# Performance work log

Hardware: AMD Instinct MI355X
Metric: run time of the kernel (lower is better)

## Reference

```python
import jax, jax.numpy as jnp
import numpy as np
import math

N_COARSE, N_FINE = 8192, 32768
DEC_DIM, ENC_DIM, OUT_DIM, K = 256, 128, 128, 16
LN_EPS = 1e-5


def setup_inputs() -> dict:
    key = jax.random.key(0)
    ks = jax.random.split(key, 16)
    s = lambda fan_in: 1.0 / math.sqrt(fan_in)
    return {
        "decoder_features": jax.random.normal(ks[0], (N_COARSE, DEC_DIM), jnp.float32),
        "decoder_pos": jax.random.normal(ks[1], (N_COARSE, 3), jnp.float32),
        "encoder_features": jax.random.normal(ks[2], (N_FINE, ENC_DIM), jnp.float32),
        "encoder_pos": jax.random.normal(ks[3], (N_FINE, 3), jnp.float32),
        "encoder_labels": jax.random.randint(ks[4], (N_FINE,), 0, 13, jnp.int64),
        # params (torch nn.Linear default init scale)
        "Wq": jax.random.uniform(ks[5], (DEC_DIM, ENC_DIM), jnp.float32, -s(ENC_DIM), s(ENC_DIM)),
        "bq": jnp.zeros((DEC_DIM,), jnp.float32),
        "Wk": jax.random.uniform(ks[6], (DEC_DIM, DEC_DIM), jnp.float32, -s(DEC_DIM), s(DEC_DIM)),
        "bk": jnp.zeros((DEC_DIM,), jnp.float32),
        "Wv": jax.random.uniform(ks[7], (DEC_DIM, DEC_DIM), jnp.float32, -s(DEC_DIM), s(DEC_DIM)),
        "bv": jnp.zeros((DEC_DIM,), jnp.float32),
        "W1": jax.random.uniform(ks[8], (OUT_DIM, DEC_DIM + ENC_DIM), jnp.float32, -s(DEC_DIM + ENC_DIM), s(DEC_DIM + ENC_DIM)),
        "b1": jnp.zeros((OUT_DIM,), jnp.float32),
        "W2": jax.random.uniform(ks[9], (OUT_DIM, OUT_DIM), jnp.float32, -s(OUT_DIM), s(OUT_DIM)),
        "b2": jnp.zeros((OUT_DIM,), jnp.float32),
        "ln_g": jnp.ones((OUT_DIM,), jnp.float32),
        "ln_b": jnp.zeros((OUT_DIM,), jnp.float32),
    }


def _knn_indices(encoder_pos, decoder_pos, k):
    # For each fine (encoder) point, k nearest coarse (decoder) points.
    # squared distances [N_fine, N_coarse]
    d2 = (
        jnp.sum(encoder_pos * encoder_pos, axis=1, keepdims=True)
        - 2.0 * encoder_pos @ decoder_pos.T
        + jnp.sum(decoder_pos * decoder_pos, axis=1)[None, :]
    )
    _, idx = jax.lax.top_k(-d2, k)  # [N_fine, K]
    return idx


def reference(decoder_features, decoder_pos, encoder_features, encoder_pos,
              encoder_labels, Wq, bq, Wk, bk, Wv, bv, W1, b1, W2, b2, ln_g, ln_b):
    idx = _knn_indices(encoder_pos, decoder_pos, K)            # [Nf, K]
    nbr = decoder_features[idx]                                 # [Nf, K, Dd]
    query = encoder_features @ Wq.T + bq                        # [Nf, Dd]
    keys = nbr @ Wk.T + bk                                      # [Nf, K, Dd]
    values = nbr @ Wv.T + bv                                    # [Nf, K, Dd]
    scores = jnp.einsum('nd,nkd->nk', query, keys) / math.sqrt(DEC_DIM)
    # segment softmax over edges grouped by fine target == softmax over K
    weights = jax.nn.softmax(scores, axis=-1)                   # [Nf, K]
    agg = jnp.einsum('nk,nkd->nd', weights, values)             # [Nf, Dd]
    combined = jnp.concatenate([agg, encoder_features], axis=-1)
    h = jax.nn.relu(combined @ W1.T + b1)
    up = h @ W2.T + b2                                          # [Nf, out]
    mu = jnp.mean(up, axis=-1, keepdims=True)
    var = jnp.var(up, axis=-1, keepdims=True)
    out = (up - mu) * jax.lax.rsqrt(var + LN_EPS) * ln_g + ln_b
    # dropout is identity in eval mode
    return (out, encoder_pos, encoder_labels)
```

## Files before the change

kernel.cpp:

```cpp
#include <hip/hip_runtime.h>
#include <hip/hip_bf16.h>

typedef __hip_bfloat16 bf16;
typedef unsigned short u16;
typedef float f32x2 __attribute__((ext_vector_type(2)));

#define NC 8192
#define NF 32768
#define KNN 16
#define FMAXV 3.402823466e+38f

__device__ __forceinline__ float bfbits2f(u16 u){
  union { unsigned u; float f; } x; x.u = ((unsigned)u) << 16; return x.f;
}
__device__ __forceinline__ float asfloat(unsigned u){
  union { unsigned u; float f; } x; x.u = u; return x.f;
}
__device__ __forceinline__ f32x2 pk_fma(f32x2 a, f32x2 b, f32x2 c){
  f32x2 d;
  asm("v_pk_fma_f32 %0, %1, %2, %3" : "=v"(d) : "v"(a), "v"(b), "v"(c));
  return d;
}

__global__ __launch_bounds__(256) void k_pw(const float* __restrict__ dpos,
                                            const float* __restrict__ W1,
                                            const float* __restrict__ W2,
                                            float4* __restrict__ posP,
                                            float4* __restrict__ W1eSa,
                                            float4* __restrict__ W1eSb,
                                            float4* __restrict__ W2Sa,
                                            float4* __restrict__ W2Sb,
                                            const float* __restrict__ Wk,
                                            const float* __restrict__ Wv,
                                            const float* __restrict__ Wq,
                                            const float* __restrict__ bk,
                                            const float* __restrict__ bv,
                                            const float* __restrict__ bq,
                                            float* __restrict__ WkqS,
                                            float* __restrict__ WvuS,
                                            float* __restrict__ bkq,
                                            float* __restrict__ bvu,
                                            float* __restrict__ wbq,
                                            float* __restrict__ sbq,
                                            const float* __restrict__ epos,
                                            const int* __restrict__ lab,
                                            float* __restrict__ out){
  __shared__ float partial[256];
  __shared__ float red[256];
  int gb = blockIdx.x, t = threadIdx.x;
  if (gb >= 1092){
    int gid = (gb - 1092) * 256 + t;
    if (gid < NF){
      float* op = out + (size_t)NF * 128;
      op[gid * 3 + 0] = epos[gid * 3 + 0];
      op[gid * 3 + 1] = epos[gid * 3 + 1];
      op[gid * 3 + 2] = epos[gid * 3 + 2];
      out[(size_t)NF * 128 + (size_t)NF * 3 + gid] = (float)lab[gid];
    }
    return;
  }
  if (gb >= 1028){
    int g = (gb - 1028) * 256 + t;
    if (g < 4096){
      const float2* dp2 = (const float2*)(dpos + (size_t)g * 6);
      float2 a = dp2[0], b = dp2[1], c = dp2[2];
      float x0 = a.x, y0 = a.y, z0 = b.x;
      float x1 = b.y, y1 = c.x, z1 = c.y;
      float dd0 = __fadd_rn(__fadd_rn(__fmul_rn(x0,x0), __fmul_rn(y0,y0)), __fmul_rn(z0,z0));
      float dd1 = __fadd_rn(__fadd_rn(__fmul_rn(x1,x1), __fmul_rn(y1,y1)), __fmul_rn(z1,z1));
      posP[g * 2]     = make_float4(x0, x1, y0, y1);
      posP[g * 2 + 1] = make_float4(z0, z1, dd0 * 0.5f, dd1 * 0.5f);
    } else if (g >= 8192 && g < 10240){
      int f = g - 8192; int c4 = f >> 6, jg = f & 63;
      W1eSa[f] = ((const float4*)(W1 + (size_t)(2 * jg) * 384 + 256))[c4];
    } else if (g >= 10240 && g < 12288){
      int f = g - 10240; int c4 = f >> 6, jg = f & 63;
      W1eSb[f] = ((const float4*)(W1 + (size_t)(2 * jg + 1) * 384 + 256))[c4];
    } else if (g >= 12288 && g < 14336){
      int f = g - 12288; int c4 = f >> 6, jg = f & 63;
      W2Sa[f] = ((const float4*)(W2 + (size_t)(2 * jg) * 128))[c4];
    } else if (g >= 14336 && g < 16384){
      int f = g - 14336; int c4 = f >> 6, jg = f & 63;
      W2Sb[f] = ((const float4*)(W2 + (size_t)(2 * jg + 1) * 128))[c4];
    }
    return;
  }
  int B = gb;
  int csel = B >> 2, tch = B & 3;
  int o = (t & 63) + tch * 64;
  int q = t >> 6;
  int j0 = q * 64;
  if (csel < 128){
    int c = csel;
    float acc = 0.f;
    for (int j = j0; j < j0 + 64; ++j)
      acc = fmaf(Wk[(size_t)j * 256 + o], Wq[(size_t)j * 128 + c], acc);
    partial[t] = acc;
    if (tch == 0) red[t] = bk[t] * Wq[(size_t)t * 128 + c];
    __syncthreads();
    if (t < 64){
      float a = partial[t] + partial[t + 64] + partial[t + 128] + partial[t + 192];
      WkqS[(size_t)((o >> 2) * 128 + c) * 4 + (o & 3)] = a;
    }
    if (tch == 0){
      for (int s = 128; s > 0; s >>= 1){ if (t < s) red[t] += red[t + s]; __syncthreads(); }
      if (t == 0) bkq[c] = red[0];
    }
  } else if (csel < 256){
    int h = csel - 128;
    float acc = 0.f;
    for (int j = j0; j < j0 + 64; ++j)
      acc = fmaf(Wv[(size_t)j * 256 + o], W1[(size_t)h * 384 + j], acc);
    partial[t] = acc;
    if (tch == 0) red[t] = bv[t] * W1[(size_t)h * 384 + t];
    __syncthreads();
    if (t < 64){
      float a = partial[t] + partial[t + 64] + partial[t + 128] + partial[t + 192];
      WvuS[(size_t)((o >> 2) * 128 + h) * 4 + (o & 3)] = a;
    }
    if (tch == 0){
      for (int s = 128; s > 0; s >>= 1){ if (t < s) red[t] += red[t + s]; __syncthreads(); }
      if (t == 0) bvu[h] = red[0];
    }
  } else {
    float acc = 0.f;
    for (int j = j0; j < j0 + 64; ++j)
      acc = fmaf(Wk[(size_t)j * 256 + o], bq[j], acc);
    partial[t] = acc;
    if (tch == 0) red[t] = bk[t] * bq[t];
    __syncthreads();
    if (t < 64){
      float a = partial[t] + partial[t + 64] + partial[t + 128] + partial[t + 192];
      wbq[o] = a;
    }
    if (tch == 0){
      for (int s = 128; s > 0; s >>= 1){ if (t < s) red[t] += red[t + s]; __syncthreads(); }
      if (t == 0) sbq[0] = red[0];
    }
  }
}

__global__ __launch_bounds__(256) void k_dk(const float* __restrict__ df,
                                            const float4* __restrict__ WkqS,
                                            const float4* __restrict__ WvuS,
                                            const float* __restrict__ bkq,
                                            const float* __restrict__ bvu,
                                            const float* __restrict__ wbq,
                                            const float* __restrict__ sbq,
                                            bf16* __restrict__ Zd, bf16* __restrict__ Ud,
                                            float* __restrict__ bqK,
                                            const float* __restrict__ epos,
                                            const float4* __restrict__ posP,
                                            int* __restrict__ knnI){
  __shared__ float dpart[8][32];
  __shared__ float smin[8 * 64];
  __shared__ float tauLDS[8];
  __shared__ int   cntL[8][4];
  __shared__ float lval[8][4][64];
  __shared__ int   lidx[8][4][64];

  int g = blockIdx.x, t = threadIdx.x;
  int m = g % 5, q5 = g / 5;
  if (m == 4){
    int g0 = q5 * 8;
    int half = __builtin_amdgcn_readfirstlane(t >> 7);
    int c = t & 127;
    const float4* W = half ? WvuS : WkqS;
    float acc[8];
    #pragma unroll
    for (int p = 0; p < 8; ++p) acc[p] = 0.f;
    for (int j4 = 0; j4 < 64; ++j4){
      float4 w = W[j4 * 128 + c];
      #pragma unroll
      for (int p = 0; p < 8; ++p){
        float4 a = ((const float4*)(df + (size_t)(g0 + p) * 256))[j4];
        acc[p] += w.x*a.x + w.y*a.y + w.z*a.z + w.w*a.w;
      }
    }
    float bias = half ? bvu[c] : bkq[c];
    bf16* dst = half ? Ud : Zd;
    #pragma unroll
    for (int p = 0; p < 8; ++p)
      dst[(size_t)(g0 + p) * 128 + c] = __float2bfloat16(acc[p] + bias);
    {
      int r = t >> 5, seg = t & 31;
      float s = 0.f;
      const float* dr = df + (size_t)(g0 + r) * 256 + seg * 8;
      const float* wq = wbq + seg * 8;
      #pragma unroll
      for (int e = 0; e < 8; ++e) s = fmaf(dr[e], wq[e], s);
      dpart[r][seg] = s;
    }
    __syncthreads();
    if (t < 8){
      float s = sbq[0];
      #pragma unroll
      for (int seg = 0; seg < 32; ++seg) s += dpart[t][seg];
      bqK[g0 + t] = s;
    }
    return;
  }

  int kb = q5 * 4 + m;
  int lane = t & 63, w = t >> 6;
  int n0 = kb * 8;
  f32x2 nex2[8], ney2[8], nez2[8];
  #pragma unroll
  for (int p = 0; p < 8; ++p){
    float nx = -epos[(n0 + p) * 3 + 0];
    float ny = -epos[(n0 + p) * 3 + 1];
    float nz = -epos[(n0 + p) * 3 + 2];
    nex2[p].x = nx; nex2[p].y = nx;
    ney2[p].x = ny; ney2[p].y = ny;
    nez2[p].x = nz; nez2[p].y = nz;
  }
  const float4* base = posP + w * 2048;

  f32x2 vmin2[8];
  #pragma unroll
  for (int p = 0; p < 8; ++p){ vmin2[p].x = FMAXV; vmin2[p].y = FMAXV; }
  #pragma unroll 4
  for (int s = 0; s < 16; ++s){
    int q2 = (s * 64 + lane) * 2;
    float4 XY = base[q2], ZW = base[q2 + 1];
    f32x2 X = {XY.x, XY.y}, Y = {XY.z, XY.w}, Z = {ZW.x, ZW.y}, W = {ZW.z, ZW.w};
    #pragma unroll
    for (int p = 0; p < 8; ++p){
      f32x2 v2 = pk_fma(nex2[p], X, W);
      v2 = pk_fma(ney2[p], Y, v2);
      v2 = pk_fma(nez2[p], Z, v2);
      vmin2[p].x = fminf(vmin2[p].x, v2.x);
      vmin2[p].y = fminf(vmin2[p].y, v2.y);
    }
  }
  float vmin[8];
  #pragma unroll
  for (int p = 0; p < 8; ++p) vmin[p] = fminf(vmin2[p].x, vmin2[p].y);

  #pragma unroll
  for (int k = 2; k <= 64; k <<= 1){
    #pragma unroll
    for (int j = k >> 1; j > 0; j >>= 1){
      bool keepmin = ((lane & j) == 0) == ((lane & k) == 0);
      #pragma unroll
      for (int p = 0; p < 8; ++p){
        float pv = __shfl_xor(vmin[p], j);
        vmin[p] = keepmin ? fminf(vmin[p], pv) : fmaxf(vmin[p], pv);
      }
    }
  }
  if (lane < 16){
    #pragma unroll
    for (int p = 0; p < 8; ++p) smin[p * 64 + w * 16 + lane] = vmin[p];
  }
  __syncthreads();

  {
    int src = (lane & 16) ? (lane ^ 15) : lane;
    float v0 = smin[(w * 2 + 0) * 64 + src];
    float v1 = smin[(w * 2 + 1) * 64 + src];
    #pragma unroll
    for (int j = 16; j > 0; j >>= 1){
      bool keepmin = ((lane & 32) == 0) == ((lane & j) == 0);
      float p0 = __shfl_xor(v0, j); v0 = keepmin ? fminf(v0, p0) : fmaxf(v0, p0);
      float p1 = __shfl_xor(v1, j); v1 = keepmin ? fminf(v1, p1) : fmaxf(v1, p1);
    }
    #pragma unroll
    for (int j = 32; j > 0; j >>= 1){
      bool keepmin = ((lane & j) == 0);
      float p0 = __shfl_xor(v0, j); v0 = keepmin ? fminf(v0, p0) : fmaxf(v0, p0);
      float p1 = __shfl_xor(v1, j); v1 = keepmin ? fminf(v1, p1) : fmaxf(v1, p1);
    }
    if (lane == 16){ tauLDS[w * 2] = v0; tauLDS[w * 2 + 1] = v1; }
  }
  __syncthreads();
  float tau0[8];
  #pragma unroll
  for (int p = 0; p < 8; ++p) tau0[p] = tauLDS[p];

  unsigned long long lmlt = (1ull << lane) - 1ull;
  int cnt[8] = {0,0,0,0,0,0,0,0};
  #pragma unroll 2
  for (int s = 0; s < 16; ++s){
    int q = s * 64 + lane;
    float4 XY = base[q * 2], ZW = base[q * 2 + 1];
    f32x2 X = {XY.x, XY.y}, Y = {XY.z, XY.w}, Z = {ZW.x, ZW.y}, W = {ZW.z, ZW.w};
    int cand0 = w * 2048 + q * 2;
    #pragma unroll
    for (int p = 0; p < 8; ++p){
      f32x2 v2 = pk_fma(nex2[p], X, W);
      v2 = pk_fma(ney2[p], Y, v2);
      v2 = pk_fma(nez2[p], Z, v2);
      bool h0 = v2.x <= tau0[p];
      bool h1 = v2.y <= tau0[p];
      unsigned long long m0 = __ballot(h0);
      unsigned long long m1 = __ballot(h1);
      if (m0 | m1){
        int base0 = cnt[p];
        int c0 = (int)__popcll(m0);
        if (h0){
          int s0 = base0 + (int)__popcll(m0 & lmlt);
          if (s0 < 64){ lval[p][w][s0] = v2.x; lidx[p][w][s0] = cand0; }
        }
        if (h1){
          int s1 = base0 + c0 + (int)__popcll(m1 & lmlt);
          if (s1 < 64){ lval[p][w][s1] = v2.y; lidx[p][w][s1] = cand0 + 1; }
        }
        cnt[p] = base0 + c0 + (int)__popcll(m1);
      }
    }
  }
  if (lane == 0){
    #pragma unroll
    for (int p = 0; p < 8; ++p) cntL[p][w] = (cnt[p] > 64) ? 64 : cnt[p];
  }
  __syncthreads();

  {
    int p0 = w * 2, p1 = w * 2 + 1;
    int nA = n0 + p0, nB = n0 + p1;
    int cA0 = cntL[p0][0], cA1 = cntL[p0][1], cA2 = cntL[p0][2], cA3 = cntL[p0][3];
    int cB0 = cntL[p1][0], cB1 = cntL[p1][1], cB2 = cntL[p1][2], cB3 = cntL[p1][3];
    int oA1 = cA0, oA2 = oA1 + cA1, oA3 = oA2 + cA2; int totA = oA3 + cA3; if (totA > 64) totA = 64;
    int oB1 = cB0, oB2 = oB1 + cB1, oB3 = oB2 + cB2; int totB = oB3 + cB3; if (totB > 64) totB = 64;
    int segA = (lane >= oA1) + (lane >= oA2) + (lane >= oA3);
    int segB = (lane >= oB1) + (lane >= oB2) + (lane >= oB3);
    int basA = segA == 0 ? 0 : (segA == 1 ? oA1 : (segA == 2 ? oA2 : oA3));
    int basB = segB == 0 ? 0 : (segB == 1 ? oB1 : (segB == 2 ? oB2 : oB3));
    float va = (lane < totA) ? lval[p0][segA][lane - basA] : FMAXV;
    int   ia = (lane < totA) ? lidx[p0][segA][lane - basA] : 0x7fffffff;
    float vb = (lane < totB) ? lval[p1][segB][lane - basB] : FMAXV;
    int   ib = (lane < totB) ? lidx[p1][segB][lane - basB] : 0x7fffffff;

    #pragma unroll
    for (int k = 2; k <= 16; k <<= 1){
      #pragma unroll
      for (int j = k >> 1; j > 0; j >>= 1){
        bool keepmin = ((lane & k) == 0) == ((lane & j) == 0);
        { float pv = __shfl_xor(va, j); int pid = __shfl_xor(ia, j);
          bool pl = (pv < va) || (pv == va && pid < ia);
          if (keepmin ? pl : !pl){ va = pv; ia = pid; } }
        { float pv = __shfl_xor(vb, j); int pid = __shfl_xor(ib, j);
          bool pl = (pv < vb) || (pv == vb && pid < ib);
          if (keepmin ? pl : !pl){ vb = pv; ib = pid; } }
      }
    }
    { float pv = __shfl_xor(va, 16); int pid = __shfl_xor(ia, 16);
      if ((pv < va) || (pv == va && pid < ia)){ va = pv; ia = pid; } }
    { float pv = __shfl_xor(vb, 16); int pid = __shfl_xor(ib, 16);
      if ((pv < vb) || (pv == vb && pid < ib)){ vb = pv; ib = pid; } }
    #pragma unroll
    for (int j = 8; j > 0; j >>= 1){
      bool keepmin = ((lane & 32) == 0) == ((lane & j) == 0);
      { float pv = __shfl_xor(va, j); int pid = __shfl_xor(ia, j);
        bool pl = (pv < va) || (pv == va && pid < ia);
        if (keepmin ? pl : !pl){ va = pv; ia = pid; } }
      { float pv = __shfl_xor(vb, j); int pid = __shfl_xor(ib, j);
        bool pl = (pv < vb) || (pv == vb && pid < ib);
        if (keepmin ? pl : !pl){ vb = pv; ib = pid; } }
    }
    { float pv = __shfl_xor(va, 32); int pid = __shfl_xor(ia, 32);
      if ((pv < va) || (pv == va && pid < ia)){ va = pv; ia = pid; } }
    { float pv = __shfl_xor(vb, 32); int pid = __shfl_xor(ib, 32);
      if ((pv < vb) || (pv == vb && pid < ib)){ vb = pv; ib = pid; } }

    if (lane < 16){
      knnI[(size_t)nA * 16 + lane] = ia;
      knnI[(size_t)nB * 16 + lane] = ib;
    }
  }
}

__global__ __launch_bounds__(256) void k_amlp(const int* __restrict__ knnI,
                                              const bf16* __restrict__ Zd,
                                              const bf16* __restrict__ Ud,
                                              const float* __restrict__ bqK,
                                              const float* __restrict__ ef,
                                              const float4* __restrict__ W1eSa,
                                              const float4* __restrict__ W1eSb,
                                              const float* __restrict__ b1,
                                              const float4* __restrict__ W2Sa,
                                              const float4* __restrict__ W2Sb,
                                              const float* __restrict__ b2,
                                              const float* __restrict__ lng, const float* __restrict__ lnb,
                                              float* __restrict__ out){
  __shared__ float haggL[16 * 128];
  __shared__ float hbuf[16 * 128];
  __shared__ float ubuf[16 * 128];
  __shared__ float stats[32];
  int t = threadIdx.x;
  int n0 = blockIdx.x * 16;
  int lane = t & 63, w = t >> 6;

  {
    int kk = lane & 15;
    int pp = w * 4 + (lane >> 4);
    int n = n0 + pp;
    int ik = knnI[(size_t)n * 16 + kk];
    float bz = bqK[ik];
    const float4* e4 = (const float4*)(ef + (size_t)n * 128 + kk * 8);
    float4 ea = e4[0], eb = e4[1];
    int gbase = lane & 48;
    int ikk[16];
    #pragma unroll
    for (int k2 = 0; k2 < 16; ++k2) ikk[k2] = __shfl(ik, gbase | k2);
    float qv[16];
    {
      uint4 zb[8];
      #pragma unroll
      for (int k2 = 0; k2 < 8; ++k2) zb[k2] = *(const uint4*)((const u16*)Zd + (size_t)ikk[k2] * 128 + kk * 8);
      #pragma unroll
      for (int k2 = 0; k2 < 8; ++k2){
        uint4 z = zb[k2];
        float s;
        s = ea.x * asfloat(z.x << 16);
        s = fmaf(ea.y, asfloat(z.x & 0xffff0000u), s);
        s = fmaf(ea.z, asfloat(z.y << 16), s);
        s = fmaf(ea.w, asfloat(z.y & 0xffff0000u), s);
        s = fmaf(eb.x, asfloat(z.z << 16), s);
        s = fmaf(eb.y, asfloat(z.z & 0xffff0000u), s);
        s = fmaf(eb.z, asfloat(z.w << 16), s);
        s = fmaf(eb.w, asfloat(z.w & 0xffff0000u), s);
        qv[k2] = s;
      }
      #pragma unroll
      for (int k2 = 0; k2 < 8; ++k2) zb[k2] = *(const uint4*)((const u16*)Zd + (size_t)ikk[8 + k2] * 128 + kk * 8);
      #pragma unroll
      for (int k2 = 0; k2 < 8; ++k2){
        uint4 z = zb[k2];
        float s;
        s = ea.x * asfloat(z.x << 16);
        s = fmaf(ea.y, asfloat(z.x & 0xffff0000u), s);
        s = fmaf(ea.z, asfloat(z.y << 16), s);
        s = fmaf(ea.w, asfloat(z.y & 0xffff0000u), s);
        s = fmaf(eb.x, asfloat(z.z << 16), s);
        s = fmaf(eb.y, asfloat(z.z & 0xffff0000u), s);
        s = fmaf(eb.z, asfloat(z.w << 16), s);
        s = fmaf(eb.w, asfloat(z.w & 0xffff0000u), s);
        qv[8 + k2] = s;
      }
    }
    bool b1v = (lane & 1) != 0, b2v = (lane & 2) != 0, b4 = (lane & 4) != 0, b8 = (lane & 8) != 0;
    float q8[8];
    #pragma unroll
    for (int j = 0; j < 8; ++j){
      float keep = b1v ? qv[2*j+1] : qv[2*j];
      float send = b1v ? qv[2*j]   : qv[2*j+1];
      q8[j] = keep + __shfl_xor(send, 1);
    }
    float q4[4];
    #pragma unroll
    for (int j = 0; j < 4; ++j){
      float keep = b2v ? q8[2*j+1] : q8[2*j];
      float send = b2v ? q8[2*j]   : q8[2*j+1];
      q4[j] = keep + __shfl_xor(send, 2);
    }
    float q2[2];
    #pragma unroll
    for (int j = 0; j < 2; ++j){
      float keep = b4 ? q4[2*j+1] : q4[2*j];
      float send = b4 ? q4[2*j]   : q4[2*j+1];
      q2[j] = keep + __shfl_xor(send, 4);
    }
    float q1;
    {
      float keep = b8 ? q2[1] : q2[0];
      float send = b8 ? q2[0] : q2[1];
      q1 = keep + __shfl_xor(send, 8);
    }
    float sc = (q1 + bz) * (1.0f / 16.0f);
    float mx = sc;
    #pragma unroll
    for (int off = 1; off < 16; off <<= 1) mx = fmaxf(mx, __shfl_xor(mx, off));
    float e = __expf(sc - mx);
    float l = e;
    #pragma unroll
    for (int off = 1; off < 16; off <<= 1) l += __shfl_xor(l, off);
    float wgt = e / l;

    float wk[16];
    #pragma unroll
    for (int k2 = 0; k2 < 16; ++k2) wk[k2] = __shfl(wgt, gbase | k2);
    float acc8[8];
    #pragma unroll
    for (int j = 0; j < 8; ++j) acc8[j] = 0.f;
    {
      uint4 ub[8];
      #pragma unroll
      for (int k2 = 0; k2 < 8; ++k2) ub[k2] = *(const uint4*)((const u16*)Ud + (size_t)ikk[k2] * 128 + kk * 8);
      #pragma unroll
      for (int k2 = 0; k2 < 8; ++k2){
        uint4 uu = ub[k2]; float wv = wk[k2];
        acc8[0] = fmaf(wv, asfloat(uu.x << 16), acc8[0]);
        acc8[1] = fmaf(wv, asfloat(uu.x & 0xffff0000u), acc8[1]);
        acc8[2] = fmaf(wv, asfloat(uu.y << 16), acc8[2]);
        acc8[3] = fmaf(wv, asfloat(uu.y & 0xffff0000u), acc8[3]);
        acc8[4] = fmaf(wv, asfloat(uu.z << 16), acc8[4]);
        acc8[5] = fmaf(wv, asfloat(uu.z & 0xffff0000u), acc8[5]);
        acc8[6] = fmaf(wv, asfloat(uu.w << 16), acc8[6]);
        acc8[7] = fmaf(wv, asfloat(uu.w & 0xffff0000u), acc8[7]);
      }
      #pragma unroll
      for (int k2 = 0; k2 < 8; ++k2) ub[k2] = *(const uint4*)((const u16*)Ud + (size_t)ikk[8 + k2] * 128 + kk * 8);
      #pragma unroll
      for (int k2 = 0; k2 < 8; ++k2){
        uint4 uu = ub[k2]; float wv = wk[8 + k2];
        acc8[0] = fmaf(wv, asfloat(uu.x << 16), acc8[0]);
        acc8[1] = fmaf(wv, asfloat(uu.x & 0xffff0000u), acc8[1]);
        acc8[2] = fmaf(wv, asfloat(uu.y << 16), acc8[2]);
        acc8[3] = fmaf(wv, asfloat(uu.y & 0xffff0000u), acc8[3]);
        acc8[4] = fmaf(wv, asfloat(uu.z << 16), acc8[4]);
        acc8[5] = fmaf(wv, asfloat(uu.z & 0xffff0000u), acc8[5]);
        acc8[6] = fmaf(wv, asfloat(uu.w << 16), acc8[6]);
        acc8[7] = fmaf(wv, asfloat(uu.w & 0xffff0000u), acc8[7]);
      }
    }
    float4* hp = (float4*)&haggL[pp * 128 + kk * 8];
    hp[0] = make_float4(acc8[0], acc8[1], acc8[2], acc8[3]);
    hp[1] = make_float4(acc8[4], acc8[5], acc8[6], acc8[7]);
  }

  int jg = t & 63;
  int pg4 = __builtin_amdgcn_readfirstlane((t >> 6) * 4);
  int j0 = jg * 2;
  float acc[2][4];
  #pragma unroll
  for (int a = 0; a < 2; ++a)
    #pragma unroll
    for (int p = 0; p < 4; ++p) acc[a][p] = 0.f;
  #pragma unroll 4
  for (int c4 = 0; c4 < 32; ++c4){
    float4 wa = W1eSa[c4 * 64 + jg];
    float4 wb = W1eSb[c4 * 64 + jg];
    #pragma unroll
    for (int p = 0; p < 4; ++p){
      float4 x = ((const float4*)(ef + (size_t)(n0 + pg4 + p) * 128))[c4];
      acc[0][p] += wa.x*x.x + wa.y*x.y + wa.z*x.z + wa.w*x.w;
      acc[1][p] += wb.x*x.x + wb.y*x.y + wb.z*x.z + wb.w*x.w;
    }
  }
  __syncthreads();
  float b1a = b1[j0], b1b = b1[j0 + 1];
  #pragma unroll
  for (int p = 0; p < 4; ++p){
    float2 hgv = *(const float2*)&haggL[(pg4 + p) * 128 + j0];
    hbuf[(pg4 + p) * 128 + j0]     = fmaxf(acc[0][p] + b1a + hgv.x, 0.f);
    hbuf[(pg4 + p) * 128 + j0 + 1] = fmaxf(acc[1][p] + b1b + hgv.y, 0.f);
  }
  __syncthreads();
  float acc2[2][4];
  #pragma unroll
  for (int a = 0; a < 2; ++a)
    #pragma unroll
    for (int p = 0; p < 4; ++p) acc2[a][p] = 0.f;
  const float4* hb4 = (const float4*)hbuf;
  #pragma unroll 4
  for (int c4 = 0; c4 < 32; ++c4){
    float4 wa = W2Sa[c4 * 64 + jg];
    float4 wb = W2Sb[c4 * 64 + jg];
    #pragma unroll
    for (int p = 0; p < 4; ++p){
      float4 x = hb4[(pg4 + p) * 32 + c4];
      acc2[0][p] += wa.x*x.x + wa.y*x.y + wa.z*x.z + wa.w*x.w;
      acc2[1][p] += wb.x*x.x + wb.y*x.y + wb.z*x.z + wb.w*x.w;
    }
  }
  float b2a = b2[j0], b2b = b2[j0 + 1];
  float u[2][4];
  #pragma unroll
  for (int p = 0; p < 4; ++p){
    u[0][p] = acc2[0][p] + b2a;
    u[1][p] = acc2[1][p] + b2b;
    ubuf[(pg4 + p) * 128 + j0]     = u[0][p];
    ubuf[(pg4 + p) * 128 + j0 + 1] = u[1][p];
  }
  __syncthreads();
  {
    int p = t >> 4, qi = t & 15;
    const float* ub = &ubuf[p * 128 + qi * 8];
    float s = 0.f, s2 = 0.f;
    #pragma unroll
    for (int e2i = 0; e2i < 8; ++e2i){ float v = ub[e2i]; s += v; s2 += v * v; }
    #pragma unroll
    for (int off = 1; off < 16; off <<= 1){ s += __shfl_xor(s, off); s2 += __shfl_xor(s2, off); }
    if (qi == 0){
      float mu = s * (1.f / 128.f);
      float var = s2 * (1.f / 128.f) - mu * mu;
      stats[p] = mu;
      stats[16 + p] = rsqrtf(fmaxf(var, 0.f) + 1e-5f);
    }
  }
  __syncthreads();
  float ga = lng[j0], gb = lng[j0 + 1];
  float ba = lnb[j0], bbv = lnb[j0 + 1];
  #pragma unroll
  for (int p = 0; p < 4; ++p){
    float mu = stats[pg4 + p], rs = stats[16 + pg4 + p];
    out[(size_t)(n0 + pg4 + p) * 128 + j0]     = (u[0][p] - mu) * rs * ga + ba;
    out[(size_t)(n0 + pg4 + p) * 128 + j0 + 1] = (u[1][p] - mu) * rs * gb + bbv;
  }
}

extern "C" void kernel_launch(void* const* d_in, const int* in_sizes, int n_in,
                              void* d_out, int out_size, void* d_ws, size_t ws_size,
                              hipStream_t stream){
  const float* df   = (const float*)d_in[0];
  const float* dpos = (const float*)d_in[1];
  const float* ef   = (const float*)d_in[2];
  const float* epos = (const float*)d_in[3];
  const int*   lab  = (const int*)d_in[4];
  const float* Wq = (const float*)d_in[5];
  const float* bq = (const float*)d_in[6];
  const float* Wk = (const float*)d_in[7];
  const float* bk = (const float*)d_in[8];
  const float* Wv = (const float*)d_in[9];
  const float* bv = (const float*)d_in[10];
  const float* W1 = (const float*)d_in[11];
  const float* b1 = (const float*)d_in[12];
  const float* W2 = (const float*)d_in[13];
  const float* b2 = (const float*)d_in[14];
  const float* lng = (const float*)d_in[15];
  const float* lnb = (const float*)d_in[16];
  float* out = (float*)d_out;

  char* wsb = (char*)d_ws;
  float4* posP  = (float4*)(wsb);
  bf16*   Zd    = (bf16*)(wsb + 131072);
  bf16*   Ud    = (bf16*)(wsb + 2228224);
  float*  bqK   = (float*)(wsb + 4325376);
  int*    knnI  = (int*)(wsb + 4358144);
  float4* W1eSa = (float4*)(wsb + 12746752);
  float4* W1eSb = (float4*)(wsb + 12779520);
  float4* W2Sa  = (float4*)(wsb + 12812288);
  float4* W2Sb  = (float4*)(wsb + 12845056);
  float*  WkqS  = (float*)(wsb + 12877824);
  float*  WvuS  = (float*)(wsb + 13008896);
  float*  bkq   = (float*)(wsb + 13139968);
  float*  bvu   = (float*)(wsb + 13140480);
  float*  wbq   = (float*)(wsb + 13140992);
  float*  sbq   = (float*)(wsb + 13142016);

  k_pw   <<<1220, 256, 0, stream>>>(dpos, W1, W2, posP, W1eSa, W1eSb, W2Sa, W2Sb,
                                    Wk, Wv, Wq, bk, bv, bq, WkqS, WvuS, bkq, bvu, wbq, sbq,
                                    epos, lab, out);
  k_dk   <<<5120, 256, 0, stream>>>(df, (const float4*)WkqS, (const float4*)WvuS, bkq, bvu, wbq, sbq,
                                    Zd, Ud, bqK, epos, posP, knnI);
  k_amlp <<<NF / 16, 256, 0, stream>>>(knnI, Zd, Ud, bqK, ef, W1eSa, W1eSb, b1, W2Sa, W2Sb, b2, lng, lnb, out);
  (void)in_sizes; (void)n_in; (void)out_size; (void)ws_size;
}
```

Measured before the change: 302.6 us.

## Move encoder-feature W1 partial GEMM into kNN kernel as extra blocks

The encoder-feature half of the first MLP layer (ef @ W1e + b1) is moved out of the final attention/MLP kernel and into the kNN/decoder kernel as two extra block types per group of seven. The result is stored to a bf16 workspace buffer, and the final kernel only loads it and adds the aggregated term. The aim is to overlap this dense GEMM with the kNN search and shorten the tail kernel. In exchange it adds a bf16 round-trip through global memory, which costs some precision and extra traffic, and it changes the grid interleaving of the kNN kernel.

After: 318.4 us. 1.05x slower.

```diff
diff --git a/kernel.cpp b/kernel.cpp
--- a/kernel.cpp
+++ b/kernel.cpp
@@ -151,7 +151,12 @@
                                             float* __restrict__ bqK,
                                             const float* __restrict__ epos,
                                             const float4* __restrict__ posP,
-                                            int* __restrict__ knnI){
+                                            int* __restrict__ knnI,
+                                            const float* __restrict__ ef,
+                                            const float4* __restrict__ W1eSa,
+                                            const float4* __restrict__ W1eSb,
+                                            const float* __restrict__ b1,
+                                            bf16* __restrict__ E1){
   __shared__ float dpart[8][32];
   __shared__ float smin[8 * 64];
   __shared__ float tauLDS[8];
@@ -160,9 +165,40 @@
   __shared__ int   lidx[8][4][64];
 
   int g = blockIdx.x, t = threadIdx.x;
-  int m = g % 5, q5 = g / 5;
+  int m = g % 7, q7 = g / 7;
+  if (m >= 5){
+    int eb = q7 * 2 + (m - 5);
+    int n0 = eb * 16;
+    int jg = t & 63;
+    int pg4 = (t >> 6) * 4;
+    int j0 = jg * 2;
+    float acc0[4], acc1[4];
+    #pragma unroll
+    for (int p = 0; p < 4; ++p){ acc0[p] = 0.f; acc1[p] = 0.f; }
+    #pragma unroll 4
+    for (int c4 = 0; c4 < 32; ++c4){
+      float4 wa = W1eSa[c4 * 64 + jg];
+      float4 wb = W1eSb[c4 * 64 + jg];
+      #pragma unroll
+      for (int p = 0; p < 4; ++p){
+        float4 x = ((const float4*)(ef + (size_t)(n0 + pg4 + p) * 128))[c4];
+        acc0[p] += wa.x*x.x + wa.y*x.y + wa.z*x.z + wa.w*x.w;
+        acc1[p] += wb.x*x.x + wb.y*x.y + wb.z*x.z + wb.w*x.w;
+      }
+    }
+    float b1a = b1[j0], b1b = b1[j0 + 1];
+    #pragma unroll
+    for (int p = 0; p < 4; ++p){
+      size_t row = (size_t)(n0 + pg4 + p);
+      bf16 ha = __float2bfloat16(acc0[p] + b1a);
+      bf16 hb = __float2bfloat16(acc1[p] + b1b);
+      ushort2 st; st.x = *(u16*)&ha; st.y = *(u16*)&hb;
+      *(ushort2*)((u16*)E1 + row * 128 + j0) = st;
+    }
+    return;
+  }
   if (m == 4){
-    int g0 = q5 * 8;
+    int g0 = q7 * 8;
     int half = __builtin_amdgcn_readfirstlane(t >> 7);
     int c = t & 127;
     const float4* W = half ? WvuS : WkqS;
@@ -201,7 +237,7 @@
     return;
   }
 
-  int kb = q5 * 4 + m;
+  int kb = q7 * 4 + m;
   int lane = t & 63, w = t >> 6;
   int n0 = kb * 8;
   f32x2 nex2[8], ney2[8], nez2[8];
@@ -376,9 +412,7 @@
                                               const bf16* __restrict__ Ud,
                                               const float* __restrict__ bqK,
                                               const float* __restrict__ ef,
-                                              const float4* __restrict__ W1eSa,
-                                              const float4* __restrict__ W1eSb,
-                                              const float* __restrict__ b1,
+                                              const bf16* __restrict__ E1,
                                               const float4* __restrict__ W2Sa,
                                               const float4* __restrict__ W2Sb,
                                               const float* __restrict__ b2,
@@ -523,29 +557,16 @@
   int jg = t & 63;
   int pg4 = __builtin_amdgcn_readfirstlane((t >> 6) * 4);
   int j0 = jg * 2;
-  float acc[2][4];
-  #pragma unroll
-  for (int a = 0; a < 2; ++a)
-    #pragma unroll
-    for (int p = 0; p < 4; ++p) acc[a][p] = 0.f;
-  #pragma unroll 4
-  for (int c4 = 0; c4 < 32; ++c4){
-    float4 wa = W1eSa[c4 * 64 + jg];
-    float4 wb = W1eSb[c4 * 64 + jg];
-    #pragma unroll
-    for (int p = 0; p < 4; ++p){
-      float4 x = ((const float4*)(ef + (size_t)(n0 + pg4 + p) * 128))[c4];
-      acc[0][p] += wa.x*x.x + wa.y*x.y + wa.z*x.z + wa.w*x.w;
-      acc[1][p] += wb.x*x.x + wb.y*x.y + wb.z*x.z + wb.w*x.w;
-    }
-  }
+  ushort2 ev[4];
+  #pragma unroll
+  for (int p = 0; p < 4; ++p)
+    ev[p] = *(const ushort2*)((const u16*)E1 + (size_t)(n0 + pg4 + p) * 128 + j0);
   __syncthreads();
-  float b1a = b1[j0], b1b = b1[j0 + 1];
   #pragma unroll
   for (int p = 0; p < 4; ++p){
     float2 hgv = *(const float2*)&haggL[(pg4 + p) * 128 + j0];
-    hbuf[(pg4 + p) * 128 + j0]     = fmaxf(acc[0][p] + b1a + hgv.x, 0.f);
-    hbuf[(pg4 + p) * 128 + j0 + 1] = fmaxf(acc[1][p] + b1b + hgv.y, 0.f);
+    hbuf[(pg4 + p) * 128 + j0]     = fmaxf(bfbits2f(ev[p].x) + hgv.x, 0.f);
+    hbuf[(pg4 + p) * 128 + j0 + 1] = fmaxf(bfbits2f(ev[p].y) + hgv.y, 0.f);
   }
   __syncthreads();
   float acc2[2][4];
@@ -629,22 +650,24 @@
   bf16*   Ud    = (bf16*)(wsb + 2228224);
   float*  bqK   = (float*)(wsb + 4325376);
   int*    knnI  = (int*)(wsb + 4358144);
-  float4* W1eSa = (float4*)(wsb + 12746752);
-  float4* W1eSb = (float4*)(wsb + 12779520);
-  float4* W2Sa  = (float4*)(wsb + 12812288);
-  float4* W2Sb  = (float4*)(wsb + 12845056);
-  float*  WkqS  = (float*)(wsb + 12877824);
-  float*  WvuS  = (float*)(wsb + 13008896);
-  float*  bkq   = (float*)(wsb + 13139968);
-  float*  bvu   = (float*)(wsb + 13140480);
-  float*  wbq   = (float*)(wsb + 13140992);
-  float*  sbq   = (float*)(wsb + 13142016);
+  bf16*   E1    = (bf16*)(wsb + 6455296);
+  float4* W1eSa = (float4*)(wsb + 14843904);
+  float4* W1eSb = (float4*)(wsb + 14876672);
+  float4* W2Sa  = (float4*)(wsb + 14909440);
+  float4* W2Sb  = (float4*)(wsb + 14942208);
+  float*  WkqS  = (float*)(wsb + 14974976);
+  float*  WvuS  = (float*)(wsb + 15106048);
+  float*  bkq   = (float*)(wsb + 15237120);
+  float*  bvu   = (float*)(wsb + 15237632);
+  float*  wbq   = (float*)(wsb + 15238144);
+  float*  sbq   = (float*)(wsb + 15239168);
 
   k_pw   <<<1220, 256, 0, stream>>>(dpos, W1, W2, posP, W1eSa, W1eSb, W2Sa, W2Sb,
                                     Wk, Wv, Wq, bk, bv, bq, WkqS, WvuS, bkq, bvu, wbq, sbq,
                                     epos, lab, out);
-  k_dk   <<<5120, 256, 0, stream>>>(df, (const float4*)WkqS, (const float4*)WvuS, bkq, bvu, wbq, sbq,
-                                    Zd, Ud, bqK, epos, posP, knnI);
-  k_amlp <<<NF / 16, 256, 0, stream>>>(knnI, Zd, Ud, bqK, ef, W1eSa, W1eSb, b1, W2Sa, W2Sb, b2, lng, lnb, out);
+  k_dk   <<<7168, 256, 0, stream>>>(df, (const float4*)WkqS, (const float4*)WvuS, bkq, bvu, wbq, sbq,
+                                    Zd, Ud, bqK, epos, posP, knnI,
+                                    ef, W1eSa, W1eSb, b1, E1);
+  k_amlp <<<NF / 16, 256, 0, stream>>>(knnI, Zd, Ud, bqK, ef, E1, W2Sa, W2Sb, b2, lng, lnb, out);
   (void)in_sizes; (void)n_in; (void)out_size; (void)ws_size;
 }
```
